# Performance work log

Measured on AMD Instinct MI355X. Metric: run time of the kernel, lower is better.

The kernel has to match this reference:

```python
import jax, jax.numpy as jnp
import numpy as np

B, L, V, H = 2, 2048, 1024, 16
HD = V // H  # head size 64
EPS = 1e-3   # keras LayerNormalization default


def setup_inputs() -> dict:
    key = jax.random.key(0)
    ks = jax.random.split(key, 10)
    scale = 1.0 / np.sqrt(V)
    return {
        "query": jax.random.normal(ks[0], (B, L, V), jnp.float32),
        "key_t": jax.random.normal(ks[1], (B, L, V), jnp.float32),
        "value": jax.random.normal(ks[2], (B, L, V), jnp.float32),
        "Wq": jax.random.normal(ks[3], (H, V, HD), jnp.float32) * scale,
        "Wk": jax.random.normal(ks[4], (H, V, HD), jnp.float32) * scale,
        "Wv": jax.random.normal(ks[5], (H, V, HD), jnp.float32) * scale,
        "gamma": jnp.ones((V,), jnp.float32),
        "beta": jnp.zeros((V,), jnp.float32),
        "query_mask": jax.random.randint(ks[6], (B, L), 0, 2, jnp.int32),
        "value_mask": jax.random.randint(ks[7], (B, L), 0, 2, jnp.int32),
    }


def reference(query, key_t, value, Wq, Wk, Wv, gamma, beta, query_mask, value_mask):
    qm = query_mask.astype(jnp.float32)  # (B,L)
    vm = value_mask.astype(jnp.float32)  # (B,L)

    # per-head no-bias Dense projections, batched over heads
    Q = jnp.einsum('blv,hvd->bhld', query, Wq)
    K = jnp.einsum('blv,hvd->bhld', key_t, Wk)
    Vh = jnp.einsum('blv,hvd->bhld', value, Wv)

    scores = jnp.einsum('bhld,bhmd->bhlm', Q, K) / jnp.sqrt(jnp.float32(HD))
    attn = jax.nn.softmax(scores, axis=-1)

    # post-softmax multiplicative masking (faithful to original)
    tri = jnp.tril(jnp.ones((L, L), jnp.float32))  # (L,L) causal
    attn = attn * tri[None, None, :, :]
    attn = attn * qm[:, None, :, None] * vm[:, None, None, :]

    heads = jnp.einsum('bhlm,bhmd->bhld', attn, Vh)
    x = heads.transpose(0, 2, 1, 3).reshape(B, L, V)  # concat heads

    # dropout is identity at inference
    y = x + query
    mu = jnp.mean(y, axis=-1, keepdims=True)
    var = jnp.mean((y - mu) ** 2, axis=-1, keepdims=True)
    return gamma * (y - mu) * jax.lax.rsqrt(var + EPS) + beta
```

## Files before the change

kernel.cpp:

```cpp
#include <hip/hip_runtime.h>
#include <math.h>

constexpr int NB = 2;
constexpr int SL = 2048;
constexpr int NV = 1024;
constexpr int NH = 16;
constexpr int DH = 64;
constexpr float LN_EPS = 1e-3f;

typedef __bf16 bf16_t;
typedef __bf16 v8bf __attribute__((ext_vector_type(8)));
typedef float  v4f  __attribute__((ext_vector_type(4)));

__device__ __forceinline__ unsigned pack_bf16(float a, float b) {
  unsigned short ua = __builtin_bit_cast(unsigned short, (bf16_t)a);
  unsigned short ub = __builtin_bit_cast(unsigned short, (bf16_t)b);
  return (unsigned)ua | ((unsigned)ub << 16);
}
__device__ __forceinline__ void async_cp16(const void* g, void* l) {
  __builtin_amdgcn_global_load_lds(
      (const __attribute__((address_space(1))) unsigned int*)g,
      (__attribute__((address_space(3))) unsigned int*)l, 16, 0, 0);
}
__device__ __forceinline__ void drain_dma() {
  asm volatile("s_waitcnt vmcnt(0)" ::: "memory");
}

__global__ __launch_bounds__(256)
void acvt(const float* __restrict__ q, const float* __restrict__ k,
          const float* __restrict__ v, bf16_t* __restrict__ oq,
          bf16_t* __restrict__ ok, bf16_t* __restrict__ ov) {
  const int z = blockIdx.y;
  const float* src = z == 0 ? q : (z == 1 ? k : v);
  bf16_t*      dst = z == 0 ? oq : (z == 1 ? ok : ov);
  const size_t i = ((size_t)blockIdx.x * 256 + threadIdx.x) * 4;
  float4 f = *(const float4*)(src + i);
  uint2 u = {pack_bf16(f.x, f.y), pack_bf16(f.z, f.w)};
  *(uint2*)(dst + i) = u;
}

__global__ __launch_bounds__(256)
void wcvt(const float* __restrict__ Wq, const float* __restrict__ Wk,
          const float* __restrict__ Wv, bf16_t* __restrict__ Wt) {
  __shared__ float ls[64][65];
  const int z = blockIdx.z;
  const float* W = z == 0 ? Wq : (z == 1 ? Wk : Wv);
  const float sc = z == 0 ? 0.125f * 1.44269504f : 1.0f;
  const int h = blockIdx.y, v0 = blockIdx.x * 64;
  const int t = threadIdx.x;
  const int rr = t >> 4, c4 = t & 15;
  const float* src = W + ((size_t)h * NV + v0) * DH;
#pragma unroll
  for (int it = 0; it < 4; ++it) {
    float4 f = *(const float4*)(src + (size_t)(rr + it * 16) * DH + c4 * 4);
    ls[rr + it * 16][c4 * 4 + 0] = f.x;
    ls[rr + it * 16][c4 * 4 + 1] = f.y;
    ls[rr + it * 16][c4 * 4 + 2] = f.z;
    ls[rr + it * 16][c4 * 4 + 3] = f.w;
  }
  __syncthreads();
  const int dd = t >> 2, vq = t & 3;
  bf16_t tmp[16];
#pragma unroll
  for (int i = 0; i < 16; ++i) tmp[i] = (bf16_t)(ls[vq * 16 + i][dd] * sc);
  bf16_t* dst = Wt + ((size_t)z * NV + h * 64 + dd) * NV + v0 + vq * 16;
  *(v8bf*)dst = *(v8bf*)&tmp[0];
  *(v8bf*)(dst + 8) = *(v8bf*)&tmp[8];
}

__global__ __launch_bounds__(256, 4)
void proj_mfma(const bf16_t* __restrict__ A0, const bf16_t* __restrict__ A1,
               const bf16_t* __restrict__ A2, const bf16_t* __restrict__ Wtb,
               const int* __restrict__ vmask,
               bf16_t* __restrict__ O0, bf16_t* __restrict__ O1,
               bf16_t* __restrict__ O2) {
  __shared__ __align__(16) bf16_t Asb[2][128 * 32];
  __shared__ __align__(16) bf16_t Wsb[2][128 * 32];

  const int z = blockIdx.z;
  const bf16_t* A   = z == 0 ? A0 : (z == 1 ? A1 : A2);
  bf16_t*       out = z == 0 ? O0 : (z == 1 ? O1 : O2);
  const bf16_t* W   = Wtb + (size_t)z * NV * NV;

  const int t = threadIdx.x, w = t >> 6, lane = t & 63;
  const int g = lane >> 4, lx = lane & 15;
  const int m0 = blockIdx.x * 128, n0 = blockIdx.y * 128;
  const int rbase = (w >> 1) * 64, cbase = (w & 1) * 64;

  const int sr = lane >> 2;
  const int sc = (lane & 3);
  auto stageA = [&](int k0, int buf) {
#pragma unroll
    for (int s = 0; s < 2; ++s) {
      const int r = w * 32 + s * 16 + sr;
      const int c = sc ^ (r & 3);
      async_cp16(A + (size_t)(m0 + r) * NV + k0 + c * 8,
                 (char*)Asb[buf] + (w * 32 + s * 16) * 64);
    }
  };
  auto stageW = [&](int k0, int buf) {
#pragma unroll
    for (int s = 0; s < 2; ++s) {
      const int r = w * 32 + s * 16 + sr;
      const int c = sc ^ (r & 3);
      async_cp16(W + (size_t)(n0 + r) * NV + k0 + c * 8,
                 (char*)Wsb[buf] + (w * 32 + s * 16) * 64);
    }
  };

  v4f acc[4][4] = {};
  stageA(0, 0);
  stageW(0, 0);

  for (int it = 0; it < 32; ++it) {
    const int buf = it & 1;
    drain_dma();
    __syncthreads();
    if (it < 31) {
      stageA((it + 1) * 32, buf ^ 1);
      stageW((it + 1) * 32, buf ^ 1);
    }
    v8bf af[4], wf[4];
#pragma unroll
    for (int rt = 0; rt < 4; ++rt) {
      const int row = rbase + rt * 16 + lx;
      af[rt] = *(const v8bf*)((const char*)Asb[buf] + row * 64 +
                              ((g ^ (row & 3)) * 16));
    }
#pragma unroll
    for (int ct = 0; ct < 4; ++ct) {
      const int row = cbase + ct * 16 + lx;
      wf[ct] = *(const v8bf*)((const char*)Wsb[buf] + row * 64 +
                              ((g ^ (row & 3)) * 16));
    }
#pragma unroll
    for (int rt = 0; rt < 4; ++rt)
#pragma unroll
      for (int ct = 0; ct < 4; ++ct)
        acc[rt][ct] = __builtin_amdgcn_mfma_f32_16x16x32_bf16(
            af[rt], wf[ct], acc[rt][ct], 0, 0, 0);
  }

  if (z < 2) {
#pragma unroll
    for (int rt = 0; rt < 4; ++rt) {
#pragma unroll
      for (int reg = 0; reg < 4; ++reg) {
        const int row = m0 + rbase + rt * 16 + g * 4 + reg;
        const int b = row >> 11, l = row & (SL - 1);
#pragma unroll
        for (int ct = 0; ct < 4; ++ct) {
          const int n = n0 + cbase + ct * 16 + lx;
          const int h = n >> 6, d = n & 63;
          out[((size_t)(b * NH + h) * SL + l) * DH + d] = (bf16_t)acc[rt][ct][reg];
        }
      }
    }
  } else {
#pragma unroll
    for (int rt = 0; rt < 4; ++rt) {
      const int row = m0 + rbase + rt * 16 + g * 4;
      const int b = row >> 11, l = row & (SL - 1);
      float vm0 = (float)vmask[b * SL + l + 0];
      float vm1 = (float)vmask[b * SL + l + 1];
      float vm2 = (float)vmask[b * SL + l + 2];
      float vm3 = (float)vmask[b * SL + l + 3];
#pragma unroll
      for (int ct = 0; ct < 4; ++ct) {
        const int n = n0 + cbase + ct * 16 + lx;
        const int h = n >> 6, d = n & 63;
        uint2 u = {pack_bf16(acc[rt][ct][0] * vm0, acc[rt][ct][1] * vm1),
                   pack_bf16(acc[rt][ct][2] * vm2, acc[rt][ct][3] * vm3)};
        *(uint2*)&out[((size_t)(b * NH + h) * DH + d) * SL + l] = u;
      }
    }
  }
}

__global__ __launch_bounds__(256, 2)
void attn_mfma(const bf16_t* __restrict__ Qg, const bf16_t* __restrict__ Kg,
               const bf16_t* __restrict__ Vtg_all, const int* __restrict__ qmask,
               float* __restrict__ Xout) {
  __shared__ __align__(16) char smem[73728];

  const int id = blockIdx.x;
  const int bh = (id & 7) | ((id >> 8) << 3);
  const int qraw = (id >> 3) & 31;
  const int qb = ((id >> 8) & 1) ? qraw : 31 - qraw;
  const int t = threadIdx.x, w = t >> 6, lane = t & 63;
  const int wq = w & 1, wm = w >> 1;
  const int g = lane >> 4, lx = lane & 15;
  const int b = bh >> 4, h = bh & 15;
  const int l0 = qb * 64;
  const int lastAct = qb;
  const int NT = SL / 64;

  char* kw = smem + w * 8192;
  char* vw = smem + 32768 + w * 8192;
  char* Pw = smem + 65536 + w * 2048;
  float* obuf = (float*)smem;
  float* sbuf = (float*)(smem + 16384);

  const bf16_t* Kb  = Kg + (size_t)bh * SL * DH;
  const bf16_t* Vtg = Vtg_all + (size_t)bh * DH * SL;

  v8bf qf[2][2];
#pragma unroll
  for (int qt = 0; qt < 2; ++qt)
#pragma unroll
    for (int ks = 0; ks < 2; ++ks)
      qf[qt][ks] = *(const v8bf*)&Qg[((size_t)bh * SL + l0 + wq * 32 + qt * 16 + lx) * DH +
                                     ks * 32 + g * 8];

  v4f O[2][4] = {};
  float suml[2] = {0.f, 0.f};

  const int sr8 = lane >> 3, sc8 = lane & 7;
  auto stageK = [&](int mb, int buf) {
#pragma unroll
    for (int s = 0; s < 4; ++s) {
      const int r = s * 8 + sr8;
      const int c = sc8 ^ (r & 7);
      async_cp16(Kb + (size_t)(mb + wm * 32 + r) * DH + c * 8,
                 kw + buf * 4096 + s * 1024);
    }
  };
  const int sr4 = lane >> 2, sc4 = lane & 3;
  auto stageV = [&](int mb, int buf) {
#pragma unroll
    for (int s = 0; s < 4; ++s) {
      const int r = s * 16 + sr4;
      const int c = sc4 ^ ((r >> 1) & 3);
      async_cp16(Vtg + (size_t)r * SL + mb + wm * 32 + c * 8,
                 vw + buf * 4096 + s * 1024);
    }
  };

  stageK(0, 0);
  stageV(0, 0);

  for (int mt = 0; mt <= lastAct; ++mt) {
    const int pb = mt & 1;
    const bool nk = (mt + 1 < NT);
    const bool nv = (mt + 1 <= lastAct);
    if (nk) stageK((mt + 1) * 64, pb ^ 1);
    if (nv) stageV((mt + 1) * 64, pb ^ 1);
    if (nk && nv)      asm volatile("s_waitcnt vmcnt(8)" ::: "memory");
    else if (nk)       asm volatile("s_waitcnt vmcnt(4)" ::: "memory");
    else               asm volatile("s_waitcnt vmcnt(0)" ::: "memory");

    v4f S[2][2];
#pragma unroll
    for (int mt2 = 0; mt2 < 2; ++mt2) {
      S[mt2][0] = (v4f){0.f, 0.f, 0.f, 0.f};
      S[mt2][1] = (v4f){0.f, 0.f, 0.f, 0.f};
    }
#pragma unroll
    for (int ks = 0; ks < 2; ++ks)
#pragma unroll
      for (int mt2 = 0; mt2 < 2; ++mt2) {
        const int lr = mt2 * 16 + lx;
        v8bf kf = *(const v8bf*)(kw + pb * 4096 + lr * 128 +
                                 (((ks * 4 + g) ^ (lx & 7)) * 16));
#pragma unroll
        for (int qt = 0; qt < 2; ++qt)
          S[mt2][qt] = __builtin_amdgcn_mfma_f32_16x16x32_bf16(
              kf, qf[qt][ks], S[mt2][qt], 0, 0, 0);
      }

    const bool diagzone = (mt == qb);
#pragma unroll
    for (int mt2 = 0; mt2 < 2; ++mt2)
#pragma unroll
      for (int qt = 0; qt < 2; ++qt) {
        float e0 = __builtin_amdgcn_exp2f(S[mt2][qt][0]);
        float e1 = __builtin_amdgcn_exp2f(S[mt2][qt][1]);
        float e2 = __builtin_amdgcn_exp2f(S[mt2][qt][2]);
        float e3 = __builtin_amdgcn_exp2f(S[mt2][qt][3]);
        suml[qt] += (e0 + e1) + (e2 + e3);
        if (diagzone) {
          const int ml = mt * 64 + wm * 32 + mt2 * 16 + g * 4;
          const int ql = l0 + wq * 32 + qt * 16 + lx;
          e0 = (ml + 0 <= ql) ? e0 : 0.f;
          e1 = (ml + 1 <= ql) ? e1 : 0.f;
          e2 = (ml + 2 <= ql) ? e2 : 0.f;
          e3 = (ml + 3 <= ql) ? e3 : 0.f;
        }
        uint2 u = {pack_bf16(e0, e1), pack_bf16(e2, e3)};
        *(uint2*)(Pw + (qt * 16 + lx) * 64 +
                  (((mt2 * 2 + (g >> 1)) ^ ((lx >> 1) & 3)) * 16) +
                  (g & 1) * 8) = u;
      }

    __builtin_amdgcn_wave_barrier();

    v8bf pf[2];
#pragma unroll
    for (int qt = 0; qt < 2; ++qt)
      pf[qt] = *(const v8bf*)(Pw + (qt * 16 + lx) * 64 +
                              ((g ^ ((lx >> 1) & 3)) * 16));
#pragma unroll
    for (int dt = 0; dt < 4; ++dt) {
      const int r = dt * 16 + lx;
      v8bf vf = *(const v8bf*)(vw + pb * 4096 + r * 64 +
                               ((g ^ ((lx >> 1) & 3)) * 16));
#pragma unroll
      for (int qt = 0; qt < 2; ++qt)
        O[qt][dt] = __builtin_amdgcn_mfma_f32_16x16x32_bf16(
            pf[qt], vf, O[qt][dt], 0, 0, 0);
    }
  }

  for (int mt = lastAct + 1; mt < NT; ++mt) {
    const int pb = mt & 1;
    const bool nk = (mt + 1 < NT);
    if (nk) {
      stageK((mt + 1) * 64, pb ^ 1);
      asm volatile("s_waitcnt vmcnt(4)" ::: "memory");
    } else {
      asm volatile("s_waitcnt vmcnt(0)" ::: "memory");
    }
    v4f S[2][2];
#pragma unroll
    for (int mt2 = 0; mt2 < 2; ++mt2) {
      S[mt2][0] = (v4f){0.f, 0.f, 0.f, 0.f};
      S[mt2][1] = (v4f){0.f, 0.f, 0.f, 0.f};
    }
#pragma unroll
    for (int ks = 0; ks < 2; ++ks)
#pragma unroll
      for (int mt2 = 0; mt2 < 2; ++mt2) {
        const int lr = mt2 * 16 + lx;
        v8bf kf = *(const v8bf*)(kw + pb * 4096 + lr * 128 +
                                 (((ks * 4 + g) ^ (lx & 7)) * 16));
#pragma unroll
        for (int qt = 0; qt < 2; ++qt)
          S[mt2][qt] = __builtin_amdgcn_mfma_f32_16x16x32_bf16(
              kf, qf[qt][ks], S[mt2][qt], 0, 0, 0);
      }
#pragma unroll
    for (int mt2 = 0; mt2 < 2; ++mt2)
#pragma unroll
      for (int qt = 0; qt < 2; ++qt)
        suml[qt] += (__builtin_amdgcn_exp2f(S[mt2][qt][0]) +
                     __builtin_amdgcn_exp2f(S[mt2][qt][1])) +
                    (__builtin_amdgcn_exp2f(S[mt2][qt][2]) +
                     __builtin_amdgcn_exp2f(S[mt2][qt][3]));
  }

  suml[0] += __shfl_xor(suml[0], 16); suml[0] += __shfl_xor(suml[0], 32);
  suml[1] += __shfl_xor(suml[1], 16); suml[1] += __shfl_xor(suml[1], 32);

  __syncthreads();
  if (g == 0) {
    sbuf[((wq * 2 + wm) * 2 + 0) * 16 + lx] = suml[0];
    sbuf[((wq * 2 + wm) * 2 + 1) * 16 + lx] = suml[1];
  }
  if (wm == 1) {
#pragma unroll
    for (int qt = 0; qt < 2; ++qt)
#pragma unroll
      for (int dt = 0; dt < 4; ++dt)
#pragma unroll
        for (int reg = 0; reg < 4; ++reg)
          obuf[wq * 2048 + (qt * 16 + g * 4 + reg) * 64 +
               ((dt * 16 + lx) ^ ((g & 1) * 16))] = O[qt][dt][reg];
  }
  __syncthreads();
  if (wm == 0) {
#pragma unroll
    for (int qt = 0; qt < 2; ++qt) {
      const float stot = suml[qt] + sbuf[((wq * 2 + 1) * 2 + qt) * 16 + lx];
#pragma unroll
      for (int reg = 0; reg < 4; ++reg) {
        const int q = l0 + wq * 32 + qt * 16 + g * 4 + reg;
        const float den = __shfl(stot, g * 4 + reg);
        const float inv = (float)qmask[b * SL + q] / den;
#pragma unroll
        for (int dt = 0; dt < 4; ++dt) {
          const float val =
              (O[qt][dt][reg] +
               obuf[wq * 2048 + (qt * 16 + g * 4 + reg) * 64 +
                    ((dt * 16 + lx) ^ ((g & 1) * 16))]) *
              inv;
          Xout[((size_t)(b * SL + q)) * NV + h * DH + dt * 16 + lx] = val;
        }
      }
    }
  }
}

__global__ __launch_bounds__(256)
void ln_kernel(const float* __restrict__ X, const float* __restrict__ query,
               const float* __restrict__ gamma, const float* __restrict__ beta,
               float* __restrict__ out) {
  const int row = blockIdx.x * 4 + (threadIdx.x >> 6);
  const int lane = threadIdx.x & 63;
  const float* xr = X + (size_t)row * NV;
  const float* qr = query + (size_t)row * NV;
  float4 y[4];
  float s = 0.f, ss = 0.f;
#pragma unroll
  for (int i = 0; i < 4; ++i) {
    const int col = lane * 4 + i * 256;
    float4 xv = *(const float4*)(xr + col);
    float4 qv = *(const float4*)(qr + col);
    y[i].x = xv.x + qv.x; y[i].y = xv.y + qv.y;
    y[i].z = xv.z + qv.z; y[i].w = xv.w + qv.w;
    s  += (y[i].x + y[i].y) + (y[i].z + y[i].w);
    ss += (y[i].x * y[i].x + y[i].y * y[i].y) +
          (y[i].z * y[i].z + y[i].w * y[i].w);
  }
#pragma unroll
  for (int off = 1; off < 64; off <<= 1) {
    s  += __shfl_xor(s, off);
    ss += __shfl_xor(ss, off);
  }
  const float mu   = s * (1.f / NV);
  const float var  = ss * (1.f / NV) - mu * mu;
  const float rstd = rsqrtf(var + LN_EPS);
#pragma unroll
  for (int i = 0; i < 4; ++i) {
    const int col = lane * 4 + i * 256;
    float4 gv = *(const float4*)(gamma + col);
    float4 bv = *(const float4*)(beta + col);
    float4 o;
    o.x = gv.x * (y[i].x - mu) * rstd + bv.x;
    o.y = gv.y * (y[i].y - mu) * rstd + bv.y;
    o.z = gv.z * (y[i].z - mu) * rstd + bv.z;
    o.w = gv.w * (y[i].w - mu) * rstd + bv.w;
    *(float4*)(out + (size_t)row * NV + col) = o;
  }
}

extern "C" void kernel_launch(void* const* d_in, const int* in_sizes, int n_in,
                              void* d_out, int out_size, void* d_ws, size_t ws_size,
                              hipStream_t stream) {
  const float* query = (const float*)d_in[0];
  const float* key_t = (const float*)d_in[1];
  const float* value = (const float*)d_in[2];
  const float* Wq    = (const float*)d_in[3];
  const float* Wk    = (const float*)d_in[4];
  const float* Wv    = (const float*)d_in[5];
  const float* gamma = (const float*)d_in[6];
  const float* beta  = (const float*)d_in[7];
  const int*   qmask = (const int*)d_in[8];
  const int*   vmask = (const int*)d_in[9];
  float* out = (float*)d_out;

  const size_t per = (size_t)NB * NH * SL * DH;
  bf16_t* Qws = (bf16_t*)d_ws;
  bf16_t* Kws = Qws + per;
  bf16_t* Vws = Kws + per;
  bf16_t* Wtb = Vws + per;
  bf16_t* Aq  = Wtb + (size_t)3 * NV * NV;
  bf16_t* Ak  = Aq + per;
  bf16_t* Av  = Ak + per;

  acvt<<<dim3((NB * SL * NV) / (256 * 4), 3), 256, 0, stream>>>(
      query, key_t, value, Aq, Ak, Av);
  wcvt<<<dim3(16, 16, 3), 256, 0, stream>>>(Wq, Wk, Wv, Wtb);
  proj_mfma<<<dim3(32, 8, 3), 256, 0, stream>>>(Aq, Ak, Av, Wtb,
                                                vmask, Qws, Kws, Vws);
  attn_mfma<<<1024, 256, 0, stream>>>(Qws, Kws, Vws, qmask, out);
  ln_kernel<<<NB * SL / 4, 256, 0, stream>>>(out, query, gamma, beta, out);
}
```

Measured before the change: 221.5 us.

## Single-buffer K/V LDS tiles with in-loop prefetch to double attention occupancy

Cuts attention LDS from 72KB to 40KB by dropping double-buffering of the K and V tiles, and raises launch bounds to four blocks per CU. Each next tile is now prefetched into the same buffer right after the current tile has been read, and LDS reads are drained first. In the tail loop the idle V buffer is reused as a second K buffer so that loop keeps double buffering. This trades less overlap of loads within a wave for more resident waves to hide latency, and the tighter register budget may cause spills.

Result: faster. 207.6 us (-6.3%).

```diff
diff --git a/kernel.cpp b/kernel.cpp
--- a/kernel.cpp
+++ b/kernel.cpp
@@ -24,6 +24,9 @@
 }
 __device__ __forceinline__ void drain_dma() {
   asm volatile("s_waitcnt vmcnt(0)" ::: "memory");
+}
+__device__ __forceinline__ void lgkm0() {
+  asm volatile("s_waitcnt lgkmcnt(0)" ::: "memory");
 }
 
 __global__ __launch_bounds__(256)
@@ -177,11 +180,11 @@
   }
 }
 
-__global__ __launch_bounds__(256, 2)
+__global__ __launch_bounds__(256, 4)
 void attn_mfma(const bf16_t* __restrict__ Qg, const bf16_t* __restrict__ Kg,
                const bf16_t* __restrict__ Vtg_all, const int* __restrict__ qmask,
                float* __restrict__ Xout) {
-  __shared__ __align__(16) char smem[73728];
+  __shared__ __align__(16) char smem[40960];
 
   const int id = blockIdx.x;
   const int bh = (id & 7) | ((id >> 8) << 3);
@@ -195,9 +198,9 @@
   const int lastAct = qb;
   const int NT = SL / 64;
 
-  char* kw = smem + w * 8192;
-  char* vw = smem + 32768 + w * 8192;
-  char* Pw = smem + 65536 + w * 2048;
+  char* kw = smem + w * 4096;
+  char* vw = smem + 16384 + w * 4096;
+  char* Pw = smem + 32768 + w * 2048;
   float* obuf = (float*)smem;
   float* sbuf = (float*)(smem + 16384);
 
@@ -216,38 +219,31 @@
   float suml[2] = {0.f, 0.f};
 
   const int sr8 = lane >> 3, sc8 = lane & 7;
-  auto stageK = [&](int mb, int buf) {
+  auto stageK = [&](int mb, char* dst) {
 #pragma unroll
     for (int s = 0; s < 4; ++s) {
       const int r = s * 8 + sr8;
       const int c = sc8 ^ (r & 7);
       async_cp16(Kb + (size_t)(mb + wm * 32 + r) * DH + c * 8,
-                 kw + buf * 4096 + s * 1024);
+                 dst + s * 1024);
     }
   };
   const int sr4 = lane >> 2, sc4 = lane & 3;
-  auto stageV = [&](int mb, int buf) {
+  auto stageV = [&](int mb) {
 #pragma unroll
     for (int s = 0; s < 4; ++s) {
       const int r = s * 16 + sr4;
       const int c = sc4 ^ ((r >> 1) & 3);
       async_cp16(Vtg + (size_t)r * SL + mb + wm * 32 + c * 8,
-                 vw + buf * 4096 + s * 1024);
+                 vw + s * 1024);
     }
   };
 
-  stageK(0, 0);
-  stageV(0, 0);
+  stageK(0, kw);
+  stageV(0);
 
   for (int mt = 0; mt <= lastAct; ++mt) {
-    const int pb = mt & 1;
-    const bool nk = (mt + 1 < NT);
-    const bool nv = (mt + 1 <= lastAct);
-    if (nk) stageK((mt + 1) * 64, pb ^ 1);
-    if (nv) stageV((mt + 1) * 64, pb ^ 1);
-    if (nk && nv)      asm volatile("s_waitcnt vmcnt(8)" ::: "memory");
-    else if (nk)       asm volatile("s_waitcnt vmcnt(4)" ::: "memory");
-    else               asm volatile("s_waitcnt vmcnt(0)" ::: "memory");
+    asm volatile("s_waitcnt vmcnt(4)" ::: "memory");
 
     v4f S[2][2];
 #pragma unroll
@@ -260,13 +256,16 @@
 #pragma unroll
       for (int mt2 = 0; mt2 < 2; ++mt2) {
         const int lr = mt2 * 16 + lx;
-        v8bf kf = *(const v8bf*)(kw + pb * 4096 + lr * 128 +
+        v8bf kf = *(const v8bf*)(kw + lr * 128 +
                                  (((ks * 4 + g) ^ (lx & 7)) * 16));
 #pragma unroll
         for (int qt = 0; qt < 2; ++qt)
           S[mt2][qt] = __builtin_amdgcn_mfma_f32_16x16x32_bf16(
               kf, qf[qt][ks], S[mt2][qt], 0, 0, 0);
       }
+
+    const bool nk = (mt + 1 < NT);
+    if (nk) { lgkm0(); stageK((mt + 1) * 64, kw); }
 
     const bool diagzone = (mt == qb);
 #pragma unroll
@@ -294,6 +293,9 @@
 
     __builtin_amdgcn_wave_barrier();
 
+    if (nk) asm volatile("s_waitcnt vmcnt(4)" ::: "memory");
+    else    asm volatile("s_waitcnt vmcnt(0)" ::: "memory");
+
     v8bf pf[2];
 #pragma unroll
     for (int qt = 0; qt < 2; ++qt)
@@ -302,20 +304,24 @@
 #pragma unroll
     for (int dt = 0; dt < 4; ++dt) {
       const int r = dt * 16 + lx;
-      v8bf vf = *(const v8bf*)(vw + pb * 4096 + r * 64 +
+      v8bf vf = *(const v8bf*)(vw + r * 64 +
                                ((g ^ ((lx >> 1) & 3)) * 16));
 #pragma unroll
       for (int qt = 0; qt < 2; ++qt)
         O[qt][dt] = __builtin_amdgcn_mfma_f32_16x16x32_bf16(
             pf[qt], vf, O[qt][dt], 0, 0, 0);
     }
+
+    if (mt + 1 <= lastAct) { lgkm0(); stageV((mt + 1) * 64); }
   }
 
   for (int mt = lastAct + 1; mt < NT; ++mt) {
-    const int pb = mt & 1;
+    char* cur = ((mt - lastAct) & 1) ? kw : vw;
+    char* nxt = ((mt - lastAct) & 1) ? vw : kw;
     const bool nk = (mt + 1 < NT);
     if (nk) {
-      stageK((mt + 1) * 64, pb ^ 1);
+      lgkm0();
+      stageK((mt + 1) * 64, nxt);
       asm volatile("s_waitcnt vmcnt(4)" ::: "memory");
     } else {
       asm volatile("s_waitcnt vmcnt(0)" ::: "memory");
@@ -331,7 +337,7 @@
 #pragma unroll
       for (int mt2 = 0; mt2 < 2; ++mt2) {
         const int lr = mt2 * 16 + lx;
-        v8bf kf = *(const v8bf*)(kw + pb * 4096 + lr * 128 +
+        v8bf kf = *(const v8bf*)(cur + lr * 128 +
                                  (((ks * 4 + g) ^ (lx & 7)) * 16));
 #pragma unroll
         for (int qt = 0; qt < 2; ++qt)
```

## Shrink attention key tile to 32, keep P in registers, raise occupancy

Applied to the files above, without the earlier changes.

The attention kernel now walks keys in 32-wide tiles instead of 64, halving the K/V staging buffers so LDS drops from 72KB to 32KB and launch bounds allow 5 blocks per CU. The P matrix no longer goes through an LDS round trip. Each lane packs its bf16 probabilities into a register operand and feeds them to a 16x16x16 MFMA against a re-laid-out V tile. It also adds s_setprio around the MFMA sections and an explicit lgkmcnt wait before re-staging. The trade is twice as many loop iterations and smaller MFMAs per iteration, in exchange for higher occupancy and less LDS traffic.

Result: faster. 212.0 us (-4.3%).

```diff
diff --git a/kernel.cpp b/kernel.cpp
--- a/kernel.cpp
+++ b/kernel.cpp
@@ -10,6 +10,7 @@
 
 typedef __bf16 bf16_t;
 typedef __bf16 v8bf __attribute__((ext_vector_type(8)));
+typedef short  v4s  __attribute__((ext_vector_type(4)));
 typedef float  v4f  __attribute__((ext_vector_type(4)));
 
 __device__ __forceinline__ unsigned pack_bf16(float a, float b) {
@@ -24,6 +25,9 @@
 }
 __device__ __forceinline__ void drain_dma() {
   asm volatile("s_waitcnt vmcnt(0)" ::: "memory");
+}
+__device__ __forceinline__ void lgkm0() {
+  asm volatile("s_waitcnt lgkmcnt(0)" ::: "memory");
 }
 
 __global__ __launch_bounds__(256)
@@ -177,11 +181,11 @@
   }
 }
 
-__global__ __launch_bounds__(256, 2)
+__global__ __launch_bounds__(256, 5)
 void attn_mfma(const bf16_t* __restrict__ Qg, const bf16_t* __restrict__ Kg,
                const bf16_t* __restrict__ Vtg_all, const int* __restrict__ qmask,
                float* __restrict__ Xout) {
-  __shared__ __align__(16) char smem[73728];
+  __shared__ __align__(16) char smem[32768];
 
   const int id = blockIdx.x;
   const int bh = (id & 7) | ((id >> 8) << 3);
@@ -192,12 +196,11 @@
   const int g = lane >> 4, lx = lane & 15;
   const int b = bh >> 4, h = bh & 15;
   const int l0 = qb * 64;
-  const int lastAct = qb;
-  const int NT = SL / 64;
-
-  char* kw = smem + w * 8192;
-  char* vw = smem + 32768 + w * 8192;
-  char* Pw = smem + 65536 + w * 2048;
+  const int lastAct = 2 * qb + 1;
+  const int NT = SL / 32;
+
+  char* kw = smem + w * 4096;
+  char* vw = smem + 16384 + w * 4096;
   float* obuf = (float*)smem;
   float* sbuf = (float*)(smem + 16384);
 
@@ -218,21 +221,21 @@
   const int sr8 = lane >> 3, sc8 = lane & 7;
   auto stageK = [&](int mb, int buf) {
 #pragma unroll
-    for (int s = 0; s < 4; ++s) {
+    for (int s = 0; s < 2; ++s) {
       const int r = s * 8 + sr8;
       const int c = sc8 ^ (r & 7);
-      async_cp16(Kb + (size_t)(mb + wm * 32 + r) * DH + c * 8,
-                 kw + buf * 4096 + s * 1024);
+      async_cp16(Kb + (size_t)(mb + wm * 16 + r) * DH + c * 8,
+                 kw + buf * 2048 + s * 1024);
     }
   };
-  const int sr4 = lane >> 2, sc4 = lane & 3;
+  const int sr2 = lane >> 1, hh = lane & 1;
   auto stageV = [&](int mb, int buf) {
 #pragma unroll
-    for (int s = 0; s < 4; ++s) {
-      const int r = s * 16 + sr4;
-      const int c = sc4 ^ ((r >> 1) & 3);
-      async_cp16(Vtg + (size_t)r * SL + mb + wm * 32 + c * 8,
-                 vw + buf * 4096 + s * 1024);
+    for (int s = 0; s < 2; ++s) {
+      const int r = s * 32 + sr2;
+      const int hp = hh ^ ((r >> 2) & 1);
+      async_cp16(Vtg + (size_t)r * SL + mb + wm * 16 + hp * 8,
+                 vw + buf * 2048 + s * 1024);
     }
   };
 
@@ -241,111 +244,98 @@
 
   for (int mt = 0; mt <= lastAct; ++mt) {
     const int pb = mt & 1;
-    const bool nk = (mt + 1 < NT);
     const bool nv = (mt + 1 <= lastAct);
-    if (nk) stageK((mt + 1) * 64, pb ^ 1);
-    if (nv) stageV((mt + 1) * 64, pb ^ 1);
-    if (nk && nv)      asm volatile("s_waitcnt vmcnt(8)" ::: "memory");
-    else if (nk)       asm volatile("s_waitcnt vmcnt(4)" ::: "memory");
-    else               asm volatile("s_waitcnt vmcnt(0)" ::: "memory");
-
-    v4f S[2][2];
-#pragma unroll
-    for (int mt2 = 0; mt2 < 2; ++mt2) {
-      S[mt2][0] = (v4f){0.f, 0.f, 0.f, 0.f};
-      S[mt2][1] = (v4f){0.f, 0.f, 0.f, 0.f};
-    }
-#pragma unroll
-    for (int ks = 0; ks < 2; ++ks)
-#pragma unroll
-      for (int mt2 = 0; mt2 < 2; ++mt2) {
-        const int lr = mt2 * 16 + lx;
-        v8bf kf = *(const v8bf*)(kw + pb * 4096 + lr * 128 +
-                                 (((ks * 4 + g) ^ (lx & 7)) * 16));
-#pragma unroll
-        for (int qt = 0; qt < 2; ++qt)
-          S[mt2][qt] = __builtin_amdgcn_mfma_f32_16x16x32_bf16(
-              kf, qf[qt][ks], S[mt2][qt], 0, 0, 0);
+    lgkm0();
+    if (nv) {
+      stageK((mt + 1) * 32, pb ^ 1);
+      stageV((mt + 1) * 32, pb ^ 1);
+      asm volatile("s_waitcnt vmcnt(4)" ::: "memory");
+    } else if (mt + 1 < NT) {
+      stageK((mt + 1) * 32, pb ^ 1);
+      asm volatile("s_waitcnt vmcnt(2)" ::: "memory");
+    } else {
+      asm volatile("s_waitcnt vmcnt(0)" ::: "memory");
+    }
+
+    v4f S[2];
+    S[0] = (v4f){0.f, 0.f, 0.f, 0.f};
+    S[1] = (v4f){0.f, 0.f, 0.f, 0.f};
+    __builtin_amdgcn_s_setprio(1);
+#pragma unroll
+    for (int ks = 0; ks < 2; ++ks) {
+      v8bf kf = *(const v8bf*)(kw + pb * 2048 + lx * 128 +
+                               (((ks * 4 + g) ^ (lx & 7)) * 16));
+#pragma unroll
+      for (int qt = 0; qt < 2; ++qt)
+        S[qt] = __builtin_amdgcn_mfma_f32_16x16x32_bf16(kf, qf[qt][ks], S[qt],
+                                                        0, 0, 0);
+    }
+    __builtin_amdgcn_s_setprio(0);
+
+    const bool diagzone = (mt >= 2 * qb);
+    v4s pa[2];
+#pragma unroll
+    for (int qt = 0; qt < 2; ++qt) {
+      float e0 = __builtin_amdgcn_exp2f(S[qt][0]);
+      float e1 = __builtin_amdgcn_exp2f(S[qt][1]);
+      float e2 = __builtin_amdgcn_exp2f(S[qt][2]);
+      float e3 = __builtin_amdgcn_exp2f(S[qt][3]);
+      suml[qt] += (e0 + e1) + (e2 + e3);
+      if (diagzone) {
+        const int ml = mt * 32 + wm * 16 + g * 4;
+        const int ql = l0 + wq * 32 + qt * 16 + lx;
+        e0 = (ml + 0 <= ql) ? e0 : 0.f;
+        e1 = (ml + 1 <= ql) ? e1 : 0.f;
+        e2 = (ml + 2 <= ql) ? e2 : 0.f;
+        e3 = (ml + 3 <= ql) ? e3 : 0.f;
       }
-
-    const bool diagzone = (mt == qb);
-#pragma unroll
-    for (int mt2 = 0; mt2 < 2; ++mt2)
-#pragma unroll
-      for (int qt = 0; qt < 2; ++qt) {
-        float e0 = __builtin_amdgcn_exp2f(S[mt2][qt][0]);
-        float e1 = __builtin_amdgcn_exp2f(S[mt2][qt][1]);
-        float e2 = __builtin_amdgcn_exp2f(S[mt2][qt][2]);
-        float e3 = __builtin_amdgcn_exp2f(S[mt2][qt][3]);
-        suml[qt] += (e0 + e1) + (e2 + e3);
-        if (diagzone) {
-          const int ml = mt * 64 + wm * 32 + mt2 * 16 + g * 4;
-          const int ql = l0 + wq * 32 + qt * 16 + lx;
-          e0 = (ml + 0 <= ql) ? e0 : 0.f;
-          e1 = (ml + 1 <= ql) ? e1 : 0.f;
-          e2 = (ml + 2 <= ql) ? e2 : 0.f;
-          e3 = (ml + 3 <= ql) ? e3 : 0.f;
-        }
-        uint2 u = {pack_bf16(e0, e1), pack_bf16(e2, e3)};
-        *(uint2*)(Pw + (qt * 16 + lx) * 64 +
-                  (((mt2 * 2 + (g >> 1)) ^ ((lx >> 1) & 3)) * 16) +
-                  (g & 1) * 8) = u;
-      }
-
-    __builtin_amdgcn_wave_barrier();
-
-    v8bf pf[2];
-#pragma unroll
-    for (int qt = 0; qt < 2; ++qt)
-      pf[qt] = *(const v8bf*)(Pw + (qt * 16 + lx) * 64 +
-                              ((g ^ ((lx >> 1) & 3)) * 16));
+      uint2 up = {pack_bf16(e0, e1), pack_bf16(e2, e3)};
+      pa[qt] = __builtin_bit_cast(v4s, up);
+    }
+
+    __builtin_amdgcn_s_setprio(1);
 #pragma unroll
     for (int dt = 0; dt < 4; ++dt) {
-      const int r = dt * 16 + lx;
-      v8bf vf = *(const v8bf*)(vw + pb * 4096 + r * 64 +
-                               ((g ^ ((lx >> 1) & 3)) * 16));
+      const int dr = dt * 16 + lx;
+      const int hp = (g >> 1) ^ ((dr >> 2) & 1);
+      v4s vf = *(const v4s*)(vw + pb * 2048 + dr * 32 + hp * 16 + (g & 1) * 8);
 #pragma unroll
       for (int qt = 0; qt < 2; ++qt)
-        O[qt][dt] = __builtin_amdgcn_mfma_f32_16x16x32_bf16(
-            pf[qt], vf, O[qt][dt], 0, 0, 0);
-    }
+        O[qt][dt] = __builtin_amdgcn_mfma_f32_16x16x16bf16_1k(
+            pa[qt], vf, O[qt][dt], 0, 0, 0);
+    }
+    __builtin_amdgcn_s_setprio(0);
   }
 
   for (int mt = lastAct + 1; mt < NT; ++mt) {
     const int pb = mt & 1;
-    const bool nk = (mt + 1 < NT);
-    if (nk) {
-      stageK((mt + 1) * 64, pb ^ 1);
-      asm volatile("s_waitcnt vmcnt(4)" ::: "memory");
+    lgkm0();
+    if (mt + 1 < NT) {
+      stageK((mt + 1) * 32, pb ^ 1);
+      asm volatile("s_waitcnt vmcnt(2)" ::: "memory");
     } else {
       asm volatile("s_waitcnt vmcnt(0)" ::: "memory");
     }
-    v4f S[2][2];
-#pragma unroll
-    for (int mt2 = 0; mt2 < 2; ++mt2) {
-      S[mt2][0] = (v4f){0.f, 0.f, 0.f, 0.f};
-      S[mt2][1] = (v4f){0.f, 0.f, 0.f, 0.f};
-    }
-#pragma unroll
-    for (int ks = 0; ks < 2; ++ks)
-#pragma unroll
-      for (int mt2 = 0; mt2 < 2; ++mt2) {
-        const int lr = mt2 * 16 + lx;
-        v8bf kf = *(const v8bf*)(kw + pb * 4096 + lr * 128 +
-                                 (((ks * 4 + g) ^ (lx & 7)) * 16));
-#pragma unroll
-        for (int qt = 0; qt < 2; ++qt)
-          S[mt2][qt] = __builtin_amdgcn_mfma_f32_16x16x32_bf16(
-              kf, qf[qt][ks], S[mt2][qt], 0, 0, 0);
-      }
-#pragma unroll
-    for (int mt2 = 0; mt2 < 2; ++mt2)
+    v4f S[2];
+    S[0] = (v4f){0.f, 0.f, 0.f, 0.f};
+    S[1] = (v4f){0.f, 0.f, 0.f, 0.f};
+    __builtin_amdgcn_s_setprio(1);
+#pragma unroll
+    for (int ks = 0; ks < 2; ++ks) {
+      v8bf kf = *(const v8bf*)(kw + pb * 2048 + lx * 128 +
+                               (((ks * 4 + g) ^ (lx & 7)) * 16));
 #pragma unroll
       for (int qt = 0; qt < 2; ++qt)
-        suml[qt] += (__builtin_amdgcn_exp2f(S[mt2][qt][0]) +
-                     __builtin_amdgcn_exp2f(S[mt2][qt][1])) +
-                    (__builtin_amdgcn_exp2f(S[mt2][qt][2]) +
-                     __builtin_amdgcn_exp2f(S[mt2][qt][3]));
+        S[qt] = __builtin_amdgcn_mfma_f32_16x16x32_bf16(kf, qf[qt][ks], S[qt],
+                                                        0, 0, 0);
+    }
+    __builtin_amdgcn_s_setprio(0);
+#pragma unroll
+    for (int qt = 0; qt < 2; ++qt)
+      suml[qt] += (__builtin_amdgcn_exp2f(S[qt][0]) +
+                   __builtin_amdgcn_exp2f(S[qt][1])) +
+                  (__builtin_amdgcn_exp2f(S[qt][2]) +
+                   __builtin_amdgcn_exp2f(S[qt][3]));
   }
 
   suml[0] += __shfl_xor(suml[0], 16); suml[0] += __shfl_xor(suml[0], 32);
```
